# Optimization experiments

Measured on AMD Instinct MI355X. Metric: run time of the kernel, lower is better.

Reference implementation:

```python
import jax, jax.numpy as jnp
import numpy as np

U, I, K = 100000, 50000, 64
N_II_LAYERS = 2
N_UI_LAYERS = 3
EPS = 1e-12  # torch F.normalize default eps


def spmm(src, dst, w, x, n):
    # out[dst] += w * x[src]  (COO sparse-dense matmul, LGConv with normalize=False)
    return jax.ops.segment_sum(x[src] * w[:, None], dst, num_segments=n)


def l2norm(x):
    # torch.nn.functional.normalize(x, p=2, dim=1)
    return x / jnp.maximum(jnp.linalg.norm(x, axis=1, keepdims=True), EPS)


def setup_inputs() -> dict:
    key = jax.random.key(0)
    ks = jax.random.split(key, 9)
    E_II, E_UI = 1600000, 4800000
    return {
        "Gu": jax.random.normal(ks[0], (U, K), dtype=jnp.float32),
        "Gi": jax.random.normal(ks[1], (I, K), dtype=jnp.float32),
        "Gis": jax.random.normal(ks[2], (I, K), dtype=jnp.float32),
        "ii_w": jax.random.uniform(ks[3], (E_II,), dtype=jnp.float32),
        "ui_w": jax.random.uniform(ks[4], (E_UI,), dtype=jnp.float32),
        "ii_src": jax.random.randint(ks[5], (E_II,), 0, I, dtype=jnp.int32),
        "ii_dst": jax.random.randint(ks[6], (E_II,), 0, I, dtype=jnp.int32),
        "ui_src": jax.random.randint(ks[7], (E_UI,), 0, U + I, dtype=jnp.int32),
        "ui_dst": jax.random.randint(ks[8], (E_UI,), 0, U + I, dtype=jnp.int32),
    }


def reference(Gu, Gi, Gis, ii_w, ui_w, ii_src, ii_dst, ui_src, ui_dst):
    # item-item propagation (n_ii_layers LGConv, no per-layer norm)
    gis = Gis
    for _ in range(N_II_LAYERS):
        gis = spmm(ii_src, ii_dst, ii_w, gis, I)
    # user-item propagation with per-layer L2 normalize
    ego = jnp.concatenate([Gu, Gi], axis=0)  # [U+I, K]
    all_emb = [ego]
    for layer in range(N_UI_LAYERS):
        all_emb.append(l2norm(spmm(ui_src, ui_dst, ui_w, all_emb[layer], U + I)))
    mean_emb = jnp.mean(jnp.stack(all_emb, axis=1), axis=1)  # [U+I, K]
    gu, gi = mean_emb[:U], mean_emb[U:]
    return gu, gi + l2norm(gis)
```

## Files before the change

kernel.cpp:

```cpp
#include <hip/hip_runtime.h>
#include <hip/hip_bf16.h>

constexpr int U_N = 100000;
constexpr int I_N = 50000;
constexpr int KDIM = 64;
constexpr float EPSF = 1e-12f;

constexpr int RPB = 256;
constexpr int BSHIFT = 8;
constexpr int CH = 16384;
constexpr int CAPB = 9216;

typedef float f4 __attribute__((ext_vector_type(4)));
typedef unsigned short u16;

__device__ inline f4 ld4(const float* p) { return *(const f4*)p; }

__device__ inline unsigned pack_bf16(float a, float b) {
    unsigned ua = __float_as_uint(a);
    unsigned ub = __float_as_uint(b);
    ua += 0x7fffu + ((ua >> 16) & 1u);
    ub += 0x7fffu + ((ub >> 16) & 1u);
    return (ua >> 16) | (ub & 0xffff0000u);
}

__device__ inline void bf8_to_f32(uint4 u, float* f) {
    unsigned w0 = u.x, w1 = u.y, w2 = u.z, w3 = u.w;
    f[0] = __uint_as_float(w0 << 16);  f[1] = __uint_as_float(w0 & 0xffff0000u);
    f[2] = __uint_as_float(w1 << 16);  f[3] = __uint_as_float(w1 & 0xffff0000u);
    f[4] = __uint_as_float(w2 << 16);  f[5] = __uint_as_float(w2 & 0xffff0000u);
    f[6] = __uint_as_float(w3 << 16);  f[7] = __uint_as_float(w3 & 0xffff0000u);
}

__global__ __launch_bounds__(1024) void bpart2_k(
        const int* __restrict__ srcU, const int* __restrict__ dstU,
        const float* __restrict__ wU, int* __restrict__ curU,
        int2* __restrict__ pairsU, int nchU, int EU,
        const int* __restrict__ srcI, const int* __restrict__ dstI,
        const float* __restrict__ wI, int* __restrict__ curI,
        int2* __restrict__ pairsI, int EI) {
    __shared__ int hist[1024];
    __shared__ int rb[1024];
    int t = threadIdx.x;
    int c = blockIdx.x;
    const int* src; const int* dst; const float* w; int* gcur; int2* pairs;
    int cb, E;
    if (c < nchU) { src = srcU; dst = dstU; w = wU; gcur = curU; pairs = pairsU;
                    cb = c * CH; E = EU; }
    else          { src = srcI; dst = dstI; w = wI; gcur = curI; pairs = pairsI;
                    cb = (c - nchU) * CH; E = EI; }
    int n = min(CH, E - cb);
    hist[t] = 0;
    __syncthreads();
    for (int j = t; j < n; j += 1024)
        atomicAdd(&hist[dst[cb + j] >> BSHIFT], 1);
    __syncthreads();
    int cnt_t = hist[t];
    if (cnt_t > 0) rb[t] = atomicAdd(&gcur[t], cnt_t);
    hist[t] = 0;
    __syncthreads();
    for (int j = t; j < n; j += 1024) {
        int i = cb + j;
        int d = dst[i];
        int b = d >> BSHIFT;
        int ew = (int)((__float_as_uint(w[i]) & 0xFFFFFF00u) | (unsigned)(d & (RPB - 1)));
        int local = atomicAdd(&hist[b], 1);
        int off = rb[b] + local;
        if (off < CAPB)
            pairs[(size_t)b * CAPB + off] = make_int2(src[i], ew);
    }
}

__global__ __launch_bounds__(1024) void bfill2_k(
        const int* __restrict__ curU, const int2* __restrict__ pairsU,
        int2* __restrict__ e2U, int2* __restrict__ rowsU, int NBu, int NRu,
        int* __restrict__ ecurU,
        const int* __restrict__ curI, const int2* __restrict__ pairsI,
        int2* __restrict__ e2I, int2* __restrict__ rowsI, int NRi,
        int* __restrict__ ecurI) {
    __shared__ int hist[RPB];
    __shared__ int pos[RPB + 1];
    __shared__ int wsums[4];
    __shared__ int sbase;
    int t = threadIdx.x;
    int b = blockIdx.x;
    const int2* pairs; int2* e2; int2* rows; const int* cur; int* ecur; int bb, Nrows;
    if (b < NBu) { pairs = pairsU; e2 = e2U; rows = rowsU; cur = curU; ecur = ecurU;
                   bb = b; Nrows = NRu; }
    else         { pairs = pairsI; e2 = e2I; rows = rowsI; cur = curI; ecur = ecurI;
                   bb = b - NBu; Nrows = NRi; }
    int cnt = min(cur[bb], CAPB);
    if (t == 0) sbase = atomicAdd(ecur, cnt);
    if (t < RPB) hist[t] = 0;
    __syncthreads();
    const int2* pb = pairs + (size_t)bb * CAPB;
    for (int i = t; i < cnt; i += 1024)
        atomicAdd(&hist[pb[i].y & (RPB - 1)], 1);
    __syncthreads();
    int v = 0, incl = 0;
    if (t < RPB) {
        v = hist[t];
        incl = v;
#pragma unroll
        for (int off = 1; off < 64; off <<= 1) {
            int nn = __shfl_up(incl, off, 64);
            if ((t & 63) >= off) incl += nn;
        }
        if ((t & 63) == 63) wsums[t >> 6] = incl;
    }
    __syncthreads();
    if (t < RPB) {
        int wexcl = 0;
        int wv = t >> 6;
        for (int k = 0; k < wv; ++k) wexcl += wsums[k];
        pos[t] = incl - v + wexcl;
    }
    if (t == 0) pos[RPB] = cnt;
    __syncthreads();
    int base = sbase;
    int r0 = bb * RPB;
    if (t < RPB) {
        int row = r0 + t;
        if (row < Nrows) rows[row] = make_int2(base + pos[t], base + pos[t + 1]);
    }
    __syncthreads();
    for (int i = t; i < cnt; i += 1024) {
        int2 pe = pb[i];
        int r = pe.y & (RPB - 1);
        int p = atomicAdd(&pos[r], 1);
        e2[base + p] = make_int2(pe.x, pe.y & ~(RPB - 1));
    }
}


__device__ inline float group8_sum(float v) {
    v += __shfl_xor(v, 1, 64);
    v += __shfl_xor(v, 2, 64);
    v += __shfl_xor(v, 4, 64);
    return v;
}

__device__ inline void spmm_row_bf(const int2* __restrict__ e2, int j0, int j1,
                                   const u16* __restrict__ x, int g, int l,
                                   float a[8]) {
    float a0[8] = {0, 0, 0, 0, 0, 0, 0, 0};
    float a1[8] = {0, 0, 0, 0, 0, 0, 0, 0};
    int j = j0;
    for (; j + 16 <= j1; j += 16) {
        int2 ea = e2[j + g];
        int2 eb = e2[j + 8 + g];
        uint4 ua = *(const uint4*)(x + (size_t)ea.x * KDIM + l * 8);
        uint4 ub = *(const uint4*)(x + (size_t)eb.x * KDIM + l * 8);
        float wa = __int_as_float(ea.y), wb = __int_as_float(eb.y);
        float fa[8], fb[8];
        bf8_to_f32(ua, fa);
        bf8_to_f32(ub, fb);
#pragma unroll
        for (int c = 0; c < 8; ++c) {
            a0[c] += wa * fa[c];
            a1[c] += wb * fb[c];
        }
    }
    for (; j < j1; j += 8) {
        if (j + g < j1) {
            int2 ea = e2[j + g];
            uint4 ua = *(const uint4*)(x + (size_t)ea.x * KDIM + l * 8);
            float wa = __int_as_float(ea.y);
            float fa[8];
            bf8_to_f32(ua, fa);
#pragma unroll
            for (int c = 0; c < 8; ++c) a0[c] += wa * fa[c];
        }
    }
#pragma unroll
    for (int c = 0; c < 8; ++c) {
        float v = a0[c] + a1[c];
        v += __shfl_xor(v, 8, 64);
        v += __shfl_xor(v, 16, 64);
        v += __shfl_xor(v, 32, 64);
        a[c] = v;
    }
}

__global__ void cvt_all(const float* __restrict__ Gu, const float* __restrict__ Gi,
                        const float* __restrict__ Gis, u16* __restrict__ bufA,
                        u16* __restrict__ gis0, int nu8, int na8, int ntot8) {
    int i = blockIdx.x * blockDim.x + threadIdx.x;
    if (i >= ntot8) return;
    const float* p;
    u16* o;
    if (i < nu8)      { p = Gu  + (size_t)i * 8;          o = bufA + (size_t)i * 8; }
    else if (i < na8) { p = Gi  + (size_t)(i - nu8) * 8;  o = bufA + (size_t)i * 8; }
    else              { p = Gis + (size_t)(i - na8) * 8;  o = gis0 + (size_t)(i - na8) * 8; }
    f4 v0 = ld4(p);
    f4 v1 = ld4(p + 4);
    uint4 pk;
    pk.x = pack_bf16(v0.x, v0.y);
    pk.y = pack_bf16(v0.z, v0.w);
    pk.z = pack_bf16(v1.x, v1.y);
    pk.w = pack_bf16(v1.z, v1.w);
    *(uint4*)o = pk;
}

__global__ void spmm_fused_l1(const int2* __restrict__ ui_rows, const int2* __restrict__ ui_e,
                              const u16* __restrict__ xu, u16* __restrict__ yu,
                              const int2* __restrict__ ii_rows, const int2* __restrict__ ii_e,
                              const u16* __restrict__ xi, u16* __restrict__ yi,
                              int nui, int nii) {
    const int lane = threadIdx.x & 63;
    const int g = lane >> 3, l = lane & 7;
    const int r = (blockIdx.x * blockDim.x + threadIdx.x) >> 6;
    if (r < nui) {
        int2 se = ui_rows[r];
        float a[8];
        spmm_row_bf(ui_e, se.x, se.y, xu, g, l, a);
        float loc = 0.f;
#pragma unroll
        for (int c = 0; c < 8; ++c) loc += a[c] * a[c];
        float ss = group8_sum(loc);
        float inv = 1.f / fmaxf(sqrtf(ss), EPSF);
        if (g == 0) {
            uint4 pk;
            pk.x = pack_bf16(a[0] * inv, a[1] * inv);
            pk.y = pack_bf16(a[2] * inv, a[3] * inv);
            pk.z = pack_bf16(a[4] * inv, a[5] * inv);
            pk.w = pack_bf16(a[6] * inv, a[7] * inv);
            *(uint4*)(yu + (size_t)r * KDIM + l * 8) = pk;
        }
    } else if (r < nui + nii) {
        int rr = r - nui;
        int2 se = ii_rows[rr];
        float a[8];
        spmm_row_bf(ii_e, se.x, se.y, xi, g, l, a);
        if (g == 0) {
            uint4 pk;
            pk.x = pack_bf16(a[0], a[1]);
            pk.y = pack_bf16(a[2], a[3]);
            pk.z = pack_bf16(a[4], a[5]);
            pk.w = pack_bf16(a[6], a[7]);
            *(uint4*)(yi + (size_t)rr * KDIM + l * 8) = pk;
        }
    }
}

__global__ void spmm_fused_l2(const int2* __restrict__ ui_rows, const int2* __restrict__ ui_e,
                              const u16* __restrict__ xu, u16* __restrict__ yu,
                              const int2* __restrict__ ii_rows, const int2* __restrict__ ii_e,
                              const u16* __restrict__ xi, float* __restrict__ yi,
                              int nui, int nii) {
    const int lane = threadIdx.x & 63;
    const int g = lane >> 3, l = lane & 7;
    const int r = (blockIdx.x * blockDim.x + threadIdx.x) >> 6;
    if (r < nui) {
        int2 se = ui_rows[r];
        float a[8];
        spmm_row_bf(ui_e, se.x, se.y, xu, g, l, a);
        float loc = 0.f;
#pragma unroll
        for (int c = 0; c < 8; ++c) loc += a[c] * a[c];
        float ss = group8_sum(loc);
        float inv = 1.f / fmaxf(sqrtf(ss), EPSF);
        if (g == 0) {
            uint4 pk;
            pk.x = pack_bf16(a[0] * inv, a[1] * inv);
            pk.y = pack_bf16(a[2] * inv, a[3] * inv);
            pk.z = pack_bf16(a[4] * inv, a[5] * inv);
            pk.w = pack_bf16(a[6] * inv, a[7] * inv);
            *(uint4*)(yu + (size_t)r * KDIM + l * 8) = pk;
        }
    } else if (r < nui + nii) {
        int rr = r - nui;
        int2 se = ii_rows[rr];
        float a[8];
        spmm_row_bf(ii_e, se.x, se.y, xi, g, l, a);
        if (g == 0) {
            float* yp = yi + (size_t)rr * KDIM + l * 8;
            *(f4*)yp = f4{a[0], a[1], a[2], a[3]};
            *(f4*)(yp + 4) = f4{a[4], a[5], a[6], a[7]};
        }
    }
}

__global__ void spmm_pull_norm_final(const int2* __restrict__ rows, const int2* __restrict__ e2,
                                     const u16* __restrict__ x,
                                     const u16* __restrict__ n1,
                                     const float* __restrict__ Gu,
                                     const float* __restrict__ Gi,
                                     const float* __restrict__ gis,
                                     float* __restrict__ out, int nrows) {
    const int lane = threadIdx.x & 63;
    const int g = lane >> 3, l = lane & 7;
    const int r = (blockIdx.x * blockDim.x + threadIdx.x) >> 6;
    if (r >= nrows) return;
    int2 se = rows[r];
    float a[8];
    spmm_row_bf(e2, se.x, se.y, x, g, l, a);
    float loc = 0.f;
#pragma unroll
    for (int c = 0; c < 8; ++c) loc += a[c] * a[c];
    float ss = group8_sum(loc);
    float inv = 1.f / fmaxf(sqrtf(ss), EPSF);
    if (g != 0) return;
    const float* ep = (r < U_N) ? Gu + (size_t)r * KDIM + l * 8
                                : Gi + (size_t)(r - U_N) * KDIM + l * 8;
    f4 e0 = __builtin_nontemporal_load((const f4*)ep);
    f4 e1 = __builtin_nontemporal_load((const f4*)(ep + 4));
    uint4 u1 = *(const uint4*)(n1 + (size_t)r * KDIM + l * 8);
    uint4 u2 = *(const uint4*)(x + (size_t)r * KDIM + l * 8);
    float f1[8], f2[8];
    bf8_to_f32(u1, f1);
    bf8_to_f32(u2, f2);
    f4 v0 = (e0 + f4{f1[0], f1[1], f1[2], f1[3]} + f4{f2[0], f2[1], f2[2], f2[3]}
                + f4{a[0] * inv, a[1] * inv, a[2] * inv, a[3] * inv}) * 0.25f;
    f4 v1 = (e1 + f4{f1[4], f1[5], f1[6], f1[7]} + f4{f2[4], f2[5], f2[6], f2[7]}
                + f4{a[4] * inv, a[5] * inv, a[6] * inv, a[7] * inv}) * 0.25f;
    if (r >= U_N) {
        const float* gp = gis + (size_t)(r - U_N) * KDIM + l * 8;
        f4 g0 = ld4(gp);
        f4 g1 = ld4(gp + 4);
        float loc2 = g0.x * g0.x + g0.y * g0.y + g0.z * g0.z + g0.w * g0.w
                   + g1.x * g1.x + g1.y * g1.y + g1.z * g1.z + g1.w * g1.w;
        float ss2 = group8_sum(loc2);
        float inv2 = 1.f / fmaxf(sqrtf(ss2), EPSF);
        v0 += g0 * inv2;
        v1 += g1 * inv2;
    }
    float* op = out + (size_t)r * KDIM + l * 8;
    __builtin_nontemporal_store(v0, (f4*)op);
    __builtin_nontemporal_store(v1, (f4*)(op + 4));
}

extern "C" void kernel_launch(void* const* d_in, const int* in_sizes, int n_in,
                              void* d_out, int out_size, void* d_ws, size_t ws_size,
                              hipStream_t stream) {
    const float* Gu     = (const float*)d_in[0];
    const float* Gi     = (const float*)d_in[1];
    const float* Gis    = (const float*)d_in[2];
    const float* ii_w   = (const float*)d_in[3];
    const float* ui_w   = (const float*)d_in[4];
    const int*   ii_src = (const int*)d_in[5];
    const int*   ii_dst = (const int*)d_in[6];
    const int*   ui_src = (const int*)d_in[7];
    const int*   ui_dst = (const int*)d_in[8];
    const int E_II = in_sizes[5];
    const int E_UI = in_sizes[7];

    const int NR    = U_N + I_N;
    const size_t NI = (size_t)I_N * KDIM;
    const size_t NA = (size_t)NR * KDIM;

    const int NB_UI = (NR + RPB - 1) / RPB;
    const int NB_II = (I_N + RPB - 1) / RPB;

    u16*  bufA = (u16*)d_ws;
    u16*  bufB = bufA + NA;
    u16*  gis0 = bufB + NA;
    u16*  gisA = gis0 + NI;
    float* gisB = (float*)(gisA + NI);
    int2*  ui_e = (int2*)(gisB + NI);
    int2*  ii_e = ui_e + E_UI;
    int2*  ui_rows = ii_e + E_II;
    int2*  ii_rows = ui_rows + NR;
    int*   curU = (int*)(ii_rows + I_N);
    int*   curI = curU + NB_UI;
    int*   ecur = curI + NB_II;

    int2* pairsU = (int2*)bufA;
    int2* pairsI = pairsU + (size_t)NB_UI * CAPB;

    float* out = (float*)d_out;

    const int nchU = (E_UI + CH - 1) / CH;
    const int nchI = (E_II + CH - 1) / CH;

    (void)hipMemsetAsync(curU, 0, (NB_UI + NB_II + 2) * sizeof(int), stream);
    bpart2_k<<<nchU + nchI, 1024, 0, stream>>>(
        ui_src, ui_dst, ui_w, curU, pairsU, nchU, E_UI,
        ii_src, ii_dst, ii_w, curI, pairsI, E_II);
    bfill2_k<<<NB_UI + NB_II, 1024, 0, stream>>>(
        curU, pairsU, ui_e, ui_rows, NB_UI, NR, ecur,
        curI, pairsI, ii_e, ii_rows, I_N, ecur + 1);

    const int nu8 = (int)((size_t)U_N * KDIM / 8);
    const int na8 = (int)(NA / 8);
    const int nt8 = (int)((NA + NI) / 8);
    cvt_all<<<(nt8 + 255) / 256, 256, 0, stream>>>(Gu, Gi, Gis, bufA, gis0, nu8, na8, nt8);

    const int NTOT = NR + I_N;
    spmm_fused_l1<<<(NTOT + 3) / 4, 256, 0, stream>>>(ui_rows, ui_e, bufA, bufB,
                                                      ii_rows, ii_e, gis0, gisA, NR, I_N);
    spmm_fused_l2<<<(NTOT + 3) / 4, 256, 0, stream>>>(ui_rows, ui_e, bufB, bufA,
                                                      ii_rows, ii_e, gisA, gisB, NR, I_N);
    spmm_pull_norm_final<<<(NR + 3) / 4, 256, 0, stream>>>(ui_rows, ui_e, bufA, bufB,
                                                           Gu, Gi, gisB, out, NR);
}
```

Measured before the change: 645.4 us.

## Replace global-atomic bucket scatter with per-chunk LDS sort and count/offset matrices

The partition kernel now sorts each edge chunk by destination bucket in LDS and writes it out contiguously, together with per-chunk bucket counts and offsets, instead of scattering pairs into global bucket slots through global atomics. The fill kernel gathers each bucket's segments from all chunks into LDS with a block-wide scan, then bins by row as before. The aim is to remove scattered global writes and global atomic contention in the CSR build. The cost is large LDS use (128KB staging in bpart) and serial per-thread gather loops in bfill, which may lower occupancy.

After: 623.2 us. -3.4%, faster.

```diff
diff --git a/kernel.cpp b/kernel.cpp
--- a/kernel.cpp
+++ b/kernel.cpp
@@ -32,31 +32,53 @@
     f[6] = __uint_as_float(w3 << 16);  f[7] = __uint_as_float(w3 & 0xffff0000u);
 }
 
+__device__ inline int block_exscan(int v, int t, int* wsum) {
+    int incl = v;
+#pragma unroll
+    for (int off = 1; off < 64; off <<= 1) {
+        int nn = __shfl_up(incl, off, 64);
+        if ((t & 63) >= off) incl += nn;
+    }
+    if ((t & 63) == 63) wsum[t >> 6] = incl;
+    __syncthreads();
+    int wex = 0;
+    int wv = t >> 6;
+    for (int k = 0; k < wv; ++k) wex += wsum[k];
+    return incl - v + wex;
+}
+
 __global__ __launch_bounds__(1024) void bpart2_k(
         const int* __restrict__ srcU, const int* __restrict__ dstU,
-        const float* __restrict__ wU, int* __restrict__ curU,
-        int2* __restrict__ pairsU, int nchU, int EU,
+        const float* __restrict__ wU, int2* __restrict__ chunkU,
+        int* __restrict__ cntUm, int* __restrict__ offUm, int nchU, int EU, int NBu,
         const int* __restrict__ srcI, const int* __restrict__ dstI,
-        const float* __restrict__ wI, int* __restrict__ curI,
-        int2* __restrict__ pairsI, int EI) {
+        const float* __restrict__ wI, int2* __restrict__ chunkI,
+        int* __restrict__ cntIm, int* __restrict__ offIm, int EI, int NBi) {
+    __shared__ int2 st[CH];
     __shared__ int hist[1024];
-    __shared__ int rb[1024];
+    __shared__ int sA[1024];
+    __shared__ int wsum[16];
     int t = threadIdx.x;
     int c = blockIdx.x;
-    const int* src; const int* dst; const float* w; int* gcur; int2* pairs;
-    int cb, E;
-    if (c < nchU) { src = srcU; dst = dstU; w = wU; gcur = curU; pairs = pairsU;
-                    cb = c * CH; E = EU; }
-    else          { src = srcI; dst = dstI; w = wI; gcur = curI; pairs = pairsI;
-                    cb = (c - nchU) * CH; E = EI; }
+    const int* src; const int* dst; const float* w; int2* chunk;
+    int* cntm; int* offm; int cb, E, NB, cidx;
+    if (c < nchU) { src = srcU; dst = dstU; w = wU; chunk = chunkU;
+                    cntm = cntUm; offm = offUm; cidx = c; cb = c * CH; E = EU; NB = NBu; }
+    else          { src = srcI; dst = dstI; w = wI; chunk = chunkI;
+                    cntm = cntIm; offm = offIm; cidx = c - nchU; cb = cidx * CH; E = EI; NB = NBi; }
     int n = min(CH, E - cb);
     hist[t] = 0;
     __syncthreads();
     for (int j = t; j < n; j += 1024)
         atomicAdd(&hist[dst[cb + j] >> BSHIFT], 1);
     __syncthreads();
-    int cnt_t = hist[t];
-    if (cnt_t > 0) rb[t] = atomicAdd(&gcur[t], cnt_t);
+    int v = hist[t];
+    int ex = block_exscan(v, t, wsum);
+    sA[t] = ex;
+    if (t < NB) {
+        cntm[(size_t)cidx * NB + t] = v;
+        offm[(size_t)cidx * NB + t] = ex;
+    }
     hist[t] = 0;
     __syncthreads();
     for (int j = t; j < n; j += 1024) {
@@ -65,56 +87,60 @@
         int b = d >> BSHIFT;
         int ew = (int)((__float_as_uint(w[i]) & 0xFFFFFF00u) | (unsigned)(d & (RPB - 1)));
         int local = atomicAdd(&hist[b], 1);
-        int off = rb[b] + local;
-        if (off < CAPB)
-            pairs[(size_t)b * CAPB + off] = make_int2(src[i], ew);
-    }
+        st[sA[b] + local] = make_int2(src[i], ew);
+    }
+    __syncthreads();
+    for (int j = t; j < n; j += 1024)
+        chunk[(size_t)cb + j] = st[j];
 }
 
 __global__ __launch_bounds__(1024) void bfill2_k(
-        const int* __restrict__ curU, const int2* __restrict__ pairsU,
+        const int2* __restrict__ chunkU, const int* __restrict__ cntUm,
+        const int* __restrict__ offUm, int nchU,
         int2* __restrict__ e2U, int2* __restrict__ rowsU, int NBu, int NRu,
         int* __restrict__ ecurU,
-        const int* __restrict__ curI, const int2* __restrict__ pairsI,
-        int2* __restrict__ e2I, int2* __restrict__ rowsI, int NRi,
+        const int2* __restrict__ chunkI, const int* __restrict__ cntIm,
+        const int* __restrict__ offIm, int nchI,
+        int2* __restrict__ e2I, int2* __restrict__ rowsI, int NBi, int NRi,
         int* __restrict__ ecurI) {
+    __shared__ int2 st[CAPB];
     __shared__ int hist[RPB];
     __shared__ int pos[RPB + 1];
-    __shared__ int wsums[4];
-    __shared__ int sbase;
+    __shared__ int wsum[16];
+    __shared__ int sbase, stot;
     int t = threadIdx.x;
     int b = blockIdx.x;
-    const int2* pairs; int2* e2; int2* rows; const int* cur; int* ecur; int bb, Nrows;
-    if (b < NBu) { pairs = pairsU; e2 = e2U; rows = rowsU; cur = curU; ecur = ecurU;
-                   bb = b; Nrows = NRu; }
-    else         { pairs = pairsI; e2 = e2I; rows = rowsI; cur = curI; ecur = ecurI;
-                   bb = b - NBu; Nrows = NRi; }
-    int cnt = min(cur[bb], CAPB);
+    const int2* chunk; const int* cntm; const int* offm; int2* e2; int2* rows;
+    int* ecur; int bb, Nrows, NB, nch;
+    if (b < NBu) { chunk = chunkU; cntm = cntUm; offm = offUm; nch = nchU;
+                   e2 = e2U; rows = rowsU; ecur = ecurU; bb = b; Nrows = NRu; NB = NBu; }
+    else         { chunk = chunkI; cntm = cntIm; offm = offIm; nch = nchI;
+                   e2 = e2I; rows = rowsI; ecur = ecurI; bb = b - NBu; Nrows = NRi; NB = NBi; }
+    int myc = 0, myloc = 0;
+    if (t < nch) {
+        myc   = cntm[(size_t)t * NB + bb];
+        myloc = offm[(size_t)t * NB + bb];
+    }
+    int mystart = block_exscan(myc, t, wsum);
+    if (t == 1023) stot = mystart;
+    __syncthreads();
+    int cnt = min(stot, CAPB);
     if (t == 0) sbase = atomicAdd(ecur, cnt);
     if (t < RPB) hist[t] = 0;
-    __syncthreads();
-    const int2* pb = pairs + (size_t)bb * CAPB;
+    if (t < nch && myc > 0) {
+        const int2* sp = chunk + (size_t)t * CH + myloc;
+        for (int k = 0; k < myc; ++k) {
+            int p = mystart + k;
+            if (p < CAPB) st[p] = sp[k];
+        }
+    }
+    __syncthreads();
     for (int i = t; i < cnt; i += 1024)
-        atomicAdd(&hist[pb[i].y & (RPB - 1)], 1);
-    __syncthreads();
-    int v = 0, incl = 0;
-    if (t < RPB) {
-        v = hist[t];
-        incl = v;
-#pragma unroll
-        for (int off = 1; off < 64; off <<= 1) {
-            int nn = __shfl_up(incl, off, 64);
-            if ((t & 63) >= off) incl += nn;
-        }
-        if ((t & 63) == 63) wsums[t >> 6] = incl;
-    }
-    __syncthreads();
-    if (t < RPB) {
-        int wexcl = 0;
-        int wv = t >> 6;
-        for (int k = 0; k < wv; ++k) wexcl += wsums[k];
-        pos[t] = incl - v + wexcl;
-    }
+        atomicAdd(&hist[st[i].y & (RPB - 1)], 1);
+    __syncthreads();
+    int hv = (t < RPB) ? hist[t] : 0;
+    int hex = block_exscan(hv, t, wsum);
+    if (t < RPB) pos[t] = hex;
     if (t == 0) pos[RPB] = cnt;
     __syncthreads();
     int base = sbase;
@@ -125,7 +151,7 @@
     }
     __syncthreads();
     for (int i = t; i < cnt; i += 1024) {
-        int2 pe = pb[i];
+        int2 pe = st[i];
         int r = pe.y & (RPB - 1);
         int p = atomicAdd(&pos[r], 1);
         e2[base + p] = make_int2(pe.x, pe.y & ~(RPB - 1));
@@ -351,6 +377,8 @@
 
     const int NB_UI = (NR + RPB - 1) / RPB;
     const int NB_II = (I_N + RPB - 1) / RPB;
+    const int nchU = (E_UI + CH - 1) / CH;
+    const int nchI = (E_II + CH - 1) / CH;
 
     u16*  bufA = (u16*)d_ws;
     u16*  bufB = bufA + NA;
@@ -361,25 +389,24 @@
     int2*  ii_e = ui_e + E_UI;
     int2*  ui_rows = ii_e + E_II;
     int2*  ii_rows = ui_rows + NR;
-    int*   curU = (int*)(ii_rows + I_N);
-    int*   curI = curU + NB_UI;
-    int*   ecur = curI + NB_II;
-
-    int2* pairsU = (int2*)bufA;
-    int2* pairsI = pairsU + (size_t)NB_UI * CAPB;
+    int*   ecur  = (int*)(ii_rows + I_N);
+    int*   cntUm = ecur + 2;
+    int*   offUm = cntUm + (size_t)nchU * NB_UI;
+    int*   cntIm = offUm + (size_t)nchU * NB_UI;
+    int*   offIm = cntIm + (size_t)nchI * NB_II;
+
+    int2* chunkU = (int2*)bufA;
+    int2* chunkI = chunkU + (size_t)nchU * CH;
 
     float* out = (float*)d_out;
 
-    const int nchU = (E_UI + CH - 1) / CH;
-    const int nchI = (E_II + CH - 1) / CH;
-
-    (void)hipMemsetAsync(curU, 0, (NB_UI + NB_II + 2) * sizeof(int), stream);
+    (void)hipMemsetAsync(ecur, 0, 2 * sizeof(int), stream);
     bpart2_k<<<nchU + nchI, 1024, 0, stream>>>(
-        ui_src, ui_dst, ui_w, curU, pairsU, nchU, E_UI,
-        ii_src, ii_dst, ii_w, curI, pairsI, E_II);
+        ui_src, ui_dst, ui_w, chunkU, cntUm, offUm, nchU, E_UI, NB_UI,
+        ii_src, ii_dst, ii_w, chunkI, cntIm, offIm, E_II, NB_II);
     bfill2_k<<<NB_UI + NB_II, 1024, 0, stream>>>(
-        curU, pairsU, ui_e, ui_rows, NB_UI, NR, ecur,
-        curI, pairsI, ii_e, ii_rows, I_N, ecur + 1);
+        chunkU, cntUm, offUm, nchU, ui_e, ui_rows, NB_UI, NR, ecur,
+        chunkI, cntIm, offIm, nchI, ii_e, ii_rows, NB_II, I_N, ecur + 1);
 
     const int nu8 = (int)((size_t)U_N * KDIM / 8);
     const int na8 = (int)(NA / 8);
```
